# Optimization experiments

Measured on AMD Instinct MI355X. Metric: run time of the kernel, lower is better.

## Reference

```python
import jax, jax.numpy as jnp
import numpy as np

B, NPTS, DIM, BOOK, NC = 64, 1024, 256, 2048, 16
EPS = 1e-10


def setup_inputs() -> dict:
    key = jax.random.key(0)
    k1, k2, k3, k4 = jax.random.split(key, 4)
    return {
        "z": jax.random.normal(k1, (B, NPTS, DIM), dtype=jnp.float32),
        "c_probs": jax.random.uniform(k2, (B, NC), dtype=jnp.float32),
        "log_param_q": jnp.zeros((1,), dtype=jnp.float32),
        "book": jax.random.normal(k3, (BOOK, DIM), dtype=jnp.float32),
        "mu": jax.random.normal(k4, (NC, NPTS, DIM), dtype=jnp.float32),
        "temperature": 1,
        "is_train": 1,
    }


def reference(z, c_probs, log_param_q, book, mu, temperature, is_train):
    # mixture of per-cluster offsets: [b,c] x [c,n,d] -> [b,n,d]
    mu_mix = jnp.einsum('bc,cnd->bnd', c_probs, mu)
    zp = z + mu_mix
    param_q = jnp.exp(log_param_q)
    precision_q = 0.5 / jnp.clip(param_q, 1e-10)  # shape [1]
    zf = zp.reshape(-1, DIM)  # [b*npts, dim]
    # squared euclidean distance via ||z||^2 + ||e||^2 - 2 z e^T
    dist = (jnp.sum(zf * zf, axis=-1, keepdims=True)
            + jnp.sum(book * book, axis=-1)
            - 2.0 * zf @ book.T)
    logits = -dist * precision_q  # [b*npts, book_size]
    # gumbel-softmax sample (fixed key for determinism)
    U = jax.random.uniform(jax.random.key(42), logits.shape, dtype=logits.dtype)
    g = -jnp.log(-jnp.log(U + EPS) + EPS)
    encodings = jax.nn.softmax((logits + g) / temperature, axis=-1)
    zq = encodings @ book  # [b*npts, dim]
    return (zq.reshape(B, -1, DIM), precision_q, logits.reshape(B, -1, BOOK), mu_mix)
```

## Files before the change

kernel.cpp:

```cpp
#include <hip/hip_runtime.h>
#include <stdint.h>

#define BB     64
#define NPTS   1024
#define DIM    256
#define BOOKN  2048
#define NC     16
#define NROWS  (BB*NPTS)
#define HALF_N 67108864u
#define HALF_ROWS 32768

#define OFF_PQ ((size_t)NROWS*DIM)
#define OFF_LG (OFF_PQ + 1)
#define OFF_MM (OFF_LG + (size_t)NROWS*BOOKN)

#define WS_RN 2048
#define WS_PQ (2048 + NROWS)
#define WS_BF 67592
#define WS_MX (WS_BF + (BOOKN*DIM)/2)
#define WS_FUSED_BYTES ((size_t)(WS_MX + NROWS) * 4)

#if defined(__has_builtin)
# if __has_builtin(__builtin_amdgcn_logf)
#  define FAST_LOG2(x) __builtin_amdgcn_logf(x)
# endif
# if __has_builtin(__builtin_amdgcn_exp2f)
#  define FAST_EXP2(x) __builtin_amdgcn_exp2f(x)
# endif
#endif
#ifndef FAST_LOG2
# define FAST_LOG2(x) log2f(x)
#endif
#ifndef FAST_EXP2
# define FAST_EXP2(x) exp2f(x)
#endif

typedef unsigned short u16;
typedef short s8v  __attribute__((ext_vector_type(8)));
typedef float f32x4 __attribute__((ext_vector_type(4)));
typedef u16  u16x4 __attribute__((ext_vector_type(4)));
typedef u16  u16x8 __attribute__((ext_vector_type(8)));

__device__ __forceinline__ u16 f2bf(float x){
  uint32_t u = __float_as_uint(x);
  return (u16)((u + 0x7fffu + ((u >> 16) & 1u)) >> 16);
}
__device__ __forceinline__ float bf2f(u16 b){
  return __uint_as_float(((uint32_t)b) << 16);
}

__device__ __forceinline__ uint32_t mf_map(float f){
  uint32_t b = __float_as_uint(f);
  return (b & 0x80000000u) ? ~b : (b | 0x80000000u);
}
__device__ __forceinline__ float mf_unmap(uint32_t u){
  uint32_t b = (u & 0x80000000u) ? (u ^ 0x80000000u) : ~u;
  return __uint_as_float(b);
}

__device__ __forceinline__ uint32_t rotl32(uint32_t x, int r){
  return (x << r) | (x >> (32 - r));
}

__device__ __forceinline__ void threefry_0_42(uint32_t x0, uint32_t x1,
                                              uint32_t& o0, uint32_t& o1){
  const uint32_t ks0 = 0u;
  const uint32_t ks1 = 42u;
  const uint32_t ks2 = 0u ^ 42u ^ 0x1BD11BDAu;
  x0 += ks0; x1 += ks1;
#define TF_R(r) { x0 += x1; x1 = rotl32(x1, r); x1 ^= x0; }
  TF_R(13) TF_R(15) TF_R(26) TF_R(6)
  x0 += ks1; x1 += ks2 + 1u;
  TF_R(17) TF_R(29) TF_R(16) TF_R(24)
  x0 += ks2; x1 += ks0 + 2u;
  TF_R(13) TF_R(15) TF_R(26) TF_R(6)
  x0 += ks0; x1 += ks1 + 3u;
  TF_R(17) TF_R(29) TF_R(16) TF_R(24)
  x0 += ks1; x1 += ks2 + 4u;
  TF_R(13) TF_R(15) TF_R(26) TF_R(6)
  x0 += ks2; x1 += ks0 + 5u;
#undef TF_R
  o0 = x0; o1 = x1;
}

__global__ __launch_bounds__(256) void k_prep(const float* __restrict__ book,
    const float* __restrict__ lpq, float* __restrict__ bn,
    float* __restrict__ ws_pq, float* __restrict__ pq_out,
    unsigned int* __restrict__ wsMax)
{
  __shared__ float red[4];
  const int j = blockIdx.x, t = threadIdx.x;
  const int gid = j*256 + t;
  if (wsMax != nullptr && gid < NROWS) wsMax[gid] = 0u;
  float v = book[(size_t)j*DIM + t];
  float s = v*v;
  #pragma unroll
  for (int o = 32; o; o >>= 1) s += __shfl_down(s, o, 64);
  const int wv = t >> 6, ln = t & 63;
  if (ln == 0) red[wv] = s;
  __syncthreads();
  if (t == 0){
    bn[j] = red[0] + red[1] + red[2] + red[3];
    if (j == 0){
      float pq = fmaxf(expf(lpq[0]), 1e-10f);
      float prec = 0.5f / pq;
      ws_pq[0] = prec;
      pq_out[0] = prec;
    }
  }
}

__global__ __launch_bounds__(256) void k_bookf(const float* __restrict__ book,
                                               u16* __restrict__ bookF,
                                               u16* __restrict__ bookR)
{
  const int tid = blockIdx.x*256 + threadIdx.x;
  {
    const int l  = tid & 63;
    const int dt = (tid >> 6) & 15;
    const int jc = tid >> 10;
    const int d  = dt*16 + (l & 15);
    const int jb = jc*32 + (l >> 4)*8;
    u16x8 v;
    #pragma unroll
    for (int e = 0; e < 8; ++e) v[e] = f2bf(book[(size_t)(jb + e)*DIM + d]);
    *(u16x8*)&bookF[(size_t)tid*8] = v;
  }
  {
    const int rr = tid >> 5;
    const int cc = (tid & 31) * 8;
    const float4 f0 = *(const float4*)&book[(size_t)rr*DIM + cc];
    const float4 f1 = *(const float4*)&book[(size_t)rr*DIM + cc + 4];
    u16x8 wv;
    wv[0] = f2bf(f0.x); wv[1] = f2bf(f0.y); wv[2] = f2bf(f0.z); wv[3] = f2bf(f0.w);
    wv[4] = f2bf(f1.x); wv[5] = f2bf(f1.y); wv[6] = f2bf(f1.z); wv[7] = f2bf(f1.w);
    *(u16x8*)&bookR[(size_t)rr*DIM + cc] = wv;
  }
}

__global__ __launch_bounds__(256) void k_mix(const float* __restrict__ z,
    const float* __restrict__ cp, const float* __restrict__ mu,
    u16* __restrict__ zpBF, float* __restrict__ mm, float* __restrict__ rn)
{
  __shared__ float s_cp[BB*NC];
  const int n  = blockIdx.x;
  const int t  = threadIdx.x;
  const int wv = t >> 6, ln = t & 63;
  for (int e = t; e < BB*NC; e += 256) s_cp[e] = cp[e];
  const int d0 = ln*4;
  float4 muv[NC];
  #pragma unroll
  for (int c = 0; c < NC; ++c)
    muv[c] = *(const float4*)&mu[(size_t)(c*NPTS + n)*DIM + d0];
  __syncthreads();
  const int b0 = blockIdx.y*32 + wv*8;
  #pragma unroll 2
  for (int bb = 0; bb < 8; ++bb){
    const int b = b0 + bb;
    const size_t idx = ((size_t)(b*NPTS + n))*DIM + d0;
    const float4 z4 = *(const float4*)&z[idx];
    float4 m4 = {0.f, 0.f, 0.f, 0.f};
    #pragma unroll
    for (int c = 0; c < NC; ++c){
      const float wgt = s_cp[b*NC + c];
      m4.x = fmaf(wgt, muv[c].x, m4.x);
      m4.y = fmaf(wgt, muv[c].y, m4.y);
      m4.z = fmaf(wgt, muv[c].z, m4.z);
      m4.w = fmaf(wgt, muv[c].w, m4.w);
    }
    float4 zp4;
    zp4.x = z4.x + m4.x; zp4.y = z4.y + m4.y;
    zp4.z = z4.z + m4.z; zp4.w = z4.w + m4.w;
    *(float4*)&mm[idx] = m4;
    u16x4 zb;
    zb[0] = f2bf(zp4.x); zb[1] = f2bf(zp4.y);
    zb[2] = f2bf(zp4.z); zb[3] = f2bf(zp4.w);
    *(u16x4*)&zpBF[idx] = zb;
    float s = zp4.x*zp4.x + zp4.y*zp4.y + zp4.z*zp4.z + zp4.w*zp4.w;
    #pragma unroll
    for (int o = 32; o; o >>= 1) s += __shfl_down(s, o, 64);
    if (ln == 0) rn[b*NPTS + n] = s;
  }
}

__global__ __launch_bounds__(256) void k_logits(const u16* __restrict__ zpBF,
    const u16* __restrict__ bookR, const float* __restrict__ rn,
    const float* __restrict__ bn, const float* __restrict__ ws_pq,
    float* __restrict__ logits, unsigned int* __restrict__ wsMax)
{
  __shared__ u16 sA[128*72];
  __shared__ u16 sB[128*72];
  const int t  = threadIdx.x;
  const int l  = t & 63;
  const int w  = t >> 6;
  const int i0 = blockIdx.y * 128;
  const int j0 = blockIdx.x * 128;
  const int wr = (w >> 1) * 64;
  const int wc = (w & 1) * 64;
  const int ll = l & 15, lh = l >> 4;

  f32x4 acc[4][4];
  #pragma unroll
  for (int m = 0; m < 4; ++m)
    #pragma unroll
    for (int n = 0; n < 4; ++n)
      acc[m][n] = (f32x4){0.f, 0.f, 0.f, 0.f};

  for (int k0 = 0; k0 < DIM; k0 += 64){
    #pragma unroll
    for (int e = 0; e < 4; ++e){
      const int idx = e*256 + t;
      const int r   = idx >> 3;
      const int c8  = (idx & 7) * 8;
      *(u16x8*)&sA[r*72 + c8] =
          *(const u16x8*)&zpBF[(size_t)(i0 + r)*DIM + k0 + c8];
      *(u16x8*)&sB[r*72 + c8] =
          *(const u16x8*)&bookR[(size_t)(j0 + r)*DIM + k0 + c8];
    }
    __syncthreads();
    #pragma unroll
    for (int kk = 0; kk < 2; ++kk){
      s8v aF[4], bF[4];
      #pragma unroll
      for (int m = 0; m < 4; ++m)
        aF[m] = *(const s8v*)&sA[(wr + m*16 + ll)*72 + kk*32 + lh*8];
      #pragma unroll
      for (int n = 0; n < 4; ++n)
        bF[n] = *(const s8v*)&sB[(wc + n*16 + ll)*72 + kk*32 + lh*8];
      #pragma unroll
      for (int m = 0; m < 4; ++m)
        #pragma unroll
        for (int n = 0; n < 4; ++n)
          acc[m][n] = __builtin_amdgcn_mfma_f32_16x16x32_bf16(aF[m], bF[n], acc[m][n], 0, 0, 0);
    }
    __syncthreads();
  }

  const float pq = ws_pq[0];
  float bnv[4];
  #pragma unroll
  for (int n = 0; n < 4; ++n) bnv[n] = bn[j0 + wc + n*16 + ll];
  #pragma unroll
  for (int m = 0; m < 4; ++m){
    #pragma unroll
    for (int r = 0; r < 4; ++r){
      const int i = i0 + wr + m*16 + lh*4 + r;
      const float rni = rn[i];
      const size_t base = (size_t)i*BOOKN + j0 + wc + ll;
      float vmax = -3.4e38f;
      #pragma unroll
      for (int n = 0; n < 4; ++n){
        const float val = -pq * (rni + bnv[n] - 2.0f*acc[m][n][r]);
        logits[base + n*16] = val;
        vmax = fmaxf(vmax, val);
      }
      if (wsMax != nullptr){
        #pragma unroll
        for (int o = 1; o < 16; o <<= 1)
          vmax = fmaxf(vmax, __shfl_xor(vmax, o, 64));
        if (ll == 0) atomicMax(&wsMax[i], mf_map(vmax));
      }
    }
  }
}

__global__ __launch_bounds__(256) void k_zq(const float* __restrict__ logits,
    const u16* __restrict__ bookF, const int* __restrict__ temp,
    const unsigned int* __restrict__ wsMax, float* __restrict__ zq)
{
  __shared__ u16 sP[64*40];
  __shared__ float sM[64];
  __shared__ float sS[64][8];
  __shared__ float sInv[64];
  const int t  = threadIdx.x;
  const int i0 = blockIdx.x * 32;
  const float tinv = 1.0f / (float)temp[0];
  const float sc = tinv * 1.44269504f;

  if (wsMax != nullptr){
    if (t < 64){
      const int gi = (t < 32) ? (i0 + t) : (i0 + t - 32 + HALF_ROWS);
      sM[t] = mf_unmap(wsMax[gi]) + 17.0f;
    }
  } else {
    const int wv = t >> 6, ln = t & 63;
    for (int rr = 0; rr < 16; ++rr){
      const int r = wv*16 + rr;
      const int gi = (r < 32) ? (i0 + r) : (i0 + r - 32 + HALF_ROWS);
      const float* row = logits + (size_t)gi*BOOKN;
      float mx = -3.4e38f;
      #pragma unroll 4
      for (int e = 0; e < 32; ++e) mx = fmaxf(mx, row[e*64 + ln]);
      #pragma unroll
      for (int o = 32; o; o >>= 1) mx = fmaxf(mx, __shfl_down(mx, o, 64));
      if (ln == 0) sM[r] = mx + 17.0f;
    }
  }
  __syncthreads();

  const int w   = t >> 6;
  const int l   = t & 63;
  const int ll  = l & 15, lh = l >> 4;
  const int srA = t >> 3;
  const int sj0 = (t & 7) * 4;
  const int giA = i0 + srA;
  const float mA = sM[srA];
  const float mB = sM[srA + 32];
  const float* rowA = logits + (size_t)giA*BOOKN;
  const float* rowB = logits + (size_t)(giA + HALF_ROWS)*BOOKN;

  f32x4 acc[4][4];
  #pragma unroll
  for (int m = 0; m < 4; ++m)
    #pragma unroll
    for (int n = 0; n < 4; ++n)
      acc[m][n] = (f32x4){0.f, 0.f, 0.f, 0.f};
  float sumA = 0.f, sumB = 0.f;

  for (int jc = 0; jc < 64; ++jc){
    const int jbase = jc*32 + sj0;
    const float4 lA4 = *(const float4*)(rowA + jbase);
    const float4 lB4 = *(const float4*)(rowB + jbase);
    const float la[4] = {lA4.x, lA4.y, lA4.z, lA4.w};
    const float lb[4] = {lB4.x, lB4.y, lB4.z, lB4.w};
    #pragma unroll
    for (int e = 0; e < 4; ++e){
      const uint32_t p = (uint32_t)(giA*BOOKN + jbase + e);
      uint32_t o0, o1;
      threefry_0_42(p, p + HALF_N, o0, o1);
      const float uA = __uint_as_float((o0 >> 9) | 0x3f800000u) - 1.0f;
      const float uB = __uint_as_float((o1 >> 9) | 0x3f800000u) - 1.0f;
      const float wAv = fmaf(-0.69314718f, FAST_LOG2(uA + 1e-10f), 1e-10f);
      const float wBv = fmaf(-0.69314718f, FAST_LOG2(uB + 1e-10f), 1e-10f);
      const float eAv = ((la[e] - mA) - 0.69314718f*FAST_LOG2(wAv)) * sc;
      const float eBv = ((lb[e] - mB) - 0.69314718f*FAST_LOG2(wBv)) * sc;
      const u16 pa = f2bf(FAST_EXP2(eAv));
      const u16 pb = f2bf(FAST_EXP2(eBv));
      sP[srA*40 + sj0 + e]        = pa;
      sP[(srA + 32)*40 + sj0 + e] = pb;
      sumA += bf2f(pa);
      sumB += bf2f(pb);
    }
    s8v bF[4];
    #pragma unroll
    for (int n = 0; n < 4; ++n)
      bF[n] = *(const s8v*)&bookF[((size_t)(jc*16 + w*4 + n)*64 + l)*8];
    __syncthreads();
    s8v aF[4];
    #pragma unroll
    for (int m = 0; m < 4; ++m)
      aF[m] = *(const s8v*)&sP[(m*16 + ll)*40 + lh*8];
    #pragma unroll
    for (int n = 0; n < 4; ++n)
      #pragma unroll
      for (int m = 0; m < 4; ++m)
        acc[m][n] = __builtin_amdgcn_mfma_f32_16x16x32_bf16(aF[m], bF[n], acc[m][n], 0, 0, 0);
    __syncthreads();
  }

  sS[srA][t & 7]      = sumA;
  sS[srA + 32][t & 7] = sumB;
  __syncthreads();
  if (t < 64){
    float s = 0.f;
    #pragma unroll
    for (int e = 0; e < 8; ++e) s += sS[t][e];
    sInv[t] = 1.0f / s;
  }
  __syncthreads();

  #pragma unroll
  for (int m = 0; m < 4; ++m){
    #pragma unroll
    for (int r = 0; r < 4; ++r){
      const int lr = m*16 + lh*4 + r;
      const int gi = (lr < 32) ? (i0 + lr) : (i0 + lr - 32 + HALF_ROWS);
      const float inv = sInv[lr];
      #pragma unroll
      for (int n = 0; n < 4; ++n)
        zq[(size_t)gi*DIM + w*64 + n*16 + ll] = acc[m][n][r] * inv;
    }
  }
}

extern "C" void kernel_launch(void* const* d_in, const int* in_sizes, int n_in,
                              void* d_out, int out_size, void* d_ws, size_t ws_size,
                              hipStream_t stream)
{
  (void)in_sizes; (void)n_in; (void)out_size;
  const float* z    = (const float*)d_in[0];
  const float* cp   = (const float*)d_in[1];
  const float* lpq  = (const float*)d_in[2];
  const float* book = (const float*)d_in[3];
  const float* mu   = (const float*)d_in[4];
  const int*   temp = (const int*)d_in[5];

  float* out = (float*)d_out;
  float* zq  = out;
  float* pqo = out + OFF_PQ;
  float* lg  = out + OFF_LG;
  float* mm  = out + OFF_MM;

  u16* zpBF  = (u16*)zq;
  u16* bookR = (u16*)zq + (size_t)NROWS*DIM;

  float* ws    = (float*)d_ws;
  float* bn    = ws;
  float* rn    = ws + WS_RN;
  float* wpq   = ws + WS_PQ;
  u16*   bookF = (u16*)(ws + WS_BF);
  unsigned int* wsMax = (ws_size >= WS_FUSED_BYTES)
                      ? (unsigned int*)(ws + WS_MX) : nullptr;

  hipLaunchKernelGGL(k_prep,   dim3(BOOKN), dim3(256), 0, stream,
                     book, lpq, bn, wpq, pqo, wsMax);
  hipLaunchKernelGGL(k_bookf,  dim3(256), dim3(256), 0, stream,
                     book, bookF, bookR);
  hipLaunchKernelGGL(k_mix,    dim3(NPTS, 2), dim3(256), 0, stream,
                     z, cp, mu, zpBF, mm, rn);
  hipLaunchKernelGGL(k_logits, dim3(BOOKN/128, NROWS/128), dim3(256), 0, stream,
                     zpBF, bookR, rn, bn, wpq, lg, wsMax);
  hipLaunchKernelGGL(k_zq,     dim3(HALF_ROWS/32), dim3(256), 0, stream,
                     lg, bookF, temp, wsMax, zq);
}
```

Baseline: 1.223 ms.

## Fuse logits GEMM, gumbel softmax and codebook GEMM into one kernel

Adds a fused kernel in which each block owns 64 rows. It computes the distance logits with MFMA against a fragment-packed bf16 codebook and writes them out while tracking the row max. A second pass recomputes the logits in LDS, applies the Gumbel noise and exp, and accumulates encodings@book directly, so the large logits tensor never has to be read back. The cost is computing the logits GEMM twice per block, and the path only runs when the workspace is large enough for the extra packed codebook.

```diff
diff --git a/kernel.cpp b/kernel.cpp
--- a/kernel.cpp
+++ b/kernel.cpp
@@ -18,7 +18,9 @@
 #define WS_PQ (2048 + NROWS)
 #define WS_BF 67592
 #define WS_MX (WS_BF + (BOOKN*DIM)/2)
+#define WS_BQ 329736
 #define WS_FUSED_BYTES ((size_t)(WS_MX + NROWS) * 4)
+#define WS_A_BYTES ((size_t)(WS_BQ + (BOOKN*DIM)/2) * 4)
 
 #if defined(__has_builtin)
 # if __has_builtin(__builtin_amdgcn_logf)
@@ -111,8 +113,7 @@
 }
 
 __global__ __launch_bounds__(256) void k_bookf(const float* __restrict__ book,
-                                               u16* __restrict__ bookF,
-                                               u16* __restrict__ bookR)
+    u16* __restrict__ bookF, u16* __restrict__ bookR, u16* __restrict__ bookQ)
 {
   const int tid = blockIdx.x*256 + threadIdx.x;
   {
@@ -126,7 +127,7 @@
     for (int e = 0; e < 8; ++e) v[e] = f2bf(book[(size_t)(jb + e)*DIM + d]);
     *(u16x8*)&bookF[(size_t)tid*8] = v;
   }
-  {
+  if (bookR != nullptr){
     const int rr = tid >> 5;
     const int cc = (tid & 31) * 8;
     const float4 f0 = *(const float4*)&book[(size_t)rr*DIM + cc];
@@ -135,6 +136,19 @@
     wv[0] = f2bf(f0.x); wv[1] = f2bf(f0.y); wv[2] = f2bf(f0.z); wv[3] = f2bf(f0.w);
     wv[4] = f2bf(f1.x); wv[5] = f2bf(f1.y); wv[6] = f2bf(f1.z); wv[7] = f2bf(f1.w);
     *(u16x8*)&bookR[(size_t)rr*DIM + cc] = wv;
+  }
+  if (bookQ != nullptr){
+    const int l  = tid & 63;
+    const int ks = (tid >> 6) & 7;
+    const int jt = tid >> 9;
+    const int row = jt*16 + (l & 15);
+    const int d0  = ks*32 + (l >> 4)*8;
+    const float4 f0 = *(const float4*)&book[(size_t)row*DIM + d0];
+    const float4 f1 = *(const float4*)&book[(size_t)row*DIM + d0 + 4];
+    u16x8 v;
+    v[0] = f2bf(f0.x); v[1] = f2bf(f0.y); v[2] = f2bf(f0.z); v[3] = f2bf(f0.w);
+    v[4] = f2bf(f1.x); v[5] = f2bf(f1.y); v[6] = f2bf(f1.z); v[7] = f2bf(f1.w);
+    *(u16x8*)&bookQ[(size_t)tid*8] = v;
   }
 }
 
@@ -172,14 +186,208 @@
     zp4.x = z4.x + m4.x; zp4.y = z4.y + m4.y;
     zp4.z = z4.z + m4.z; zp4.w = z4.w + m4.w;
     *(float4*)&mm[idx] = m4;
-    u16x4 zb;
-    zb[0] = f2bf(zp4.x); zb[1] = f2bf(zp4.y);
-    zb[2] = f2bf(zp4.z); zb[3] = f2bf(zp4.w);
-    *(u16x4*)&zpBF[idx] = zb;
+    if (zpBF != nullptr){
+      u16x4 zb;
+      zb[0] = f2bf(zp4.x); zb[1] = f2bf(zp4.y);
+      zb[2] = f2bf(zp4.z); zb[3] = f2bf(zp4.w);
+      *(u16x4*)&zpBF[idx] = zb;
+    }
     float s = zp4.x*zp4.x + zp4.y*zp4.y + zp4.z*zp4.z + zp4.w*zp4.w;
     #pragma unroll
     for (int o = 32; o; o >>= 1) s += __shfl_down(s, o, 64);
     if (ln == 0) rn[b*NPTS + n] = s;
+  }
+}
+
+#define SLP 36
+__global__ __launch_bounds__(256) void k_fused(const float* __restrict__ z,
+    const float* __restrict__ mm, const float* __restrict__ rn,
+    const float* __restrict__ bn, const float* __restrict__ ws_pq,
+    const u16* __restrict__ bookQ, const u16* __restrict__ bookF,
+    const int* __restrict__ temp, float* __restrict__ logits,
+    float* __restrict__ zq)
+{
+  __shared__ u16 sQ[2][8192];
+  __shared__ float sL[64*SLP];
+  __shared__ u16 sP[64*40];
+  __shared__ float sM[64];
+  __shared__ float sS[64][8];
+  __shared__ float sInv[64];
+
+  const int t  = threadIdx.x;
+  const int w  = t >> 6;
+  const int l  = t & 63;
+  const int ll = l & 15, lh = l >> 4;
+  const int i0p = blockIdx.x * 32;
+  const float pq = ws_pq[0];
+  const float tinv = 1.0f / (float)temp[0];
+  const float sc = tinv * 1.44269504f;
+
+  const int sArow = w*16 + ll;
+  const int giA_r = (sArow < 32) ? (i0p + sArow) : (i0p + sArow - 32 + HALF_ROWS);
+  s8v aF[8];
+  #pragma unroll
+  for (int ks = 0; ks < 8; ++ks){
+    const size_t base = (size_t)giA_r*DIM + ks*32 + lh*8;
+    const float4 z0 = *(const float4*)&z[base];
+    const float4 z1 = *(const float4*)&z[base + 4];
+    const float4 m0 = *(const float4*)&mm[base];
+    const float4 m1 = *(const float4*)&mm[base + 4];
+    s8v v;
+    v[0] = f2bf(z0.x + m0.x); v[1] = f2bf(z0.y + m0.y);
+    v[2] = f2bf(z0.z + m0.z); v[3] = f2bf(z0.w + m0.w);
+    v[4] = f2bf(z1.x + m1.x); v[5] = f2bf(z1.y + m1.y);
+    v[6] = f2bf(z1.z + m1.z); v[7] = f2bf(z1.w + m1.w);
+    aF[ks] = v;
+  }
+  float rnv[4]; int giC[4];
+  #pragma unroll
+  for (int r = 0; r < 4; ++r){
+    const int s = w*16 + lh*4 + r;
+    giC[r] = (s < 32) ? (i0p + s) : (i0p + s - 32 + HALF_ROWS);
+    rnv[r] = rn[giC[r]];
+  }
+
+  float vmax[4] = {-3.4e38f, -3.4e38f, -3.4e38f, -3.4e38f};
+  for (int jc = 0; jc < 64; ++jc){
+    u16* q = sQ[jc & 1];
+    #pragma unroll
+    for (int e = 0; e < 4; ++e){
+      const int off = (e*256 + t)*8;
+      *(u16x8*)&q[off] = *(const u16x8*)&bookQ[(size_t)jc*8192 + off];
+    }
+    __syncthreads();
+    f32x4 accS[2];
+    accS[0] = (f32x4){0.f,0.f,0.f,0.f};
+    accS[1] = (f32x4){0.f,0.f,0.f,0.f};
+    #pragma unroll
+    for (int n = 0; n < 2; ++n)
+      #pragma unroll
+      for (int ks = 0; ks < 8; ++ks)
+        accS[n] = __builtin_amdgcn_mfma_f32_16x16x32_bf16(
+            aF[ks], *(const s8v*)&q[((n*8 + ks)*64 + l)*8], accS[n], 0, 0, 0);
+    const float bnv[2] = { bn[jc*32 + ll], bn[jc*32 + 16 + ll] };
+    #pragma unroll
+    for (int n = 0; n < 2; ++n)
+      #pragma unroll
+      for (int r = 0; r < 4; ++r){
+        const float val = -pq * (rnv[r] + bnv[n] - 2.0f*accS[n][r]);
+        logits[(size_t)giC[r]*BOOKN + jc*32 + n*16 + ll] = val;
+        vmax[r] = fmaxf(vmax[r], val);
+      }
+  }
+  #pragma unroll
+  for (int r = 0; r < 4; ++r){
+    float m = vmax[r];
+    #pragma unroll
+    for (int o = 1; o < 16; o <<= 1) m = fmaxf(m, __shfl_xor(m, o, 64));
+    if (ll == 0) sM[w*16 + lh*4 + r] = m + 17.0f;
+  }
+  __syncthreads();
+
+  const int srA = t >> 3;
+  const int sj0 = (t & 7) * 4;
+  const int giA = i0p + srA;
+  const float mA = sM[srA];
+  const float mB = sM[srA + 32];
+
+  f32x4 acc[4][4];
+  #pragma unroll
+  for (int m = 0; m < 4; ++m)
+    #pragma unroll
+    for (int n = 0; n < 4; ++n)
+      acc[m][n] = (f32x4){0.f, 0.f, 0.f, 0.f};
+  float sumA = 0.f, sumB = 0.f;
+
+  for (int jc = 0; jc < 64; ++jc){
+    u16* q = sQ[jc & 1];
+    #pragma unroll
+    for (int e = 0; e < 4; ++e){
+      const int off = (e*256 + t)*8;
+      *(u16x8*)&q[off] = *(const u16x8*)&bookQ[(size_t)jc*8192 + off];
+    }
+    __syncthreads();
+    f32x4 accS[2];
+    accS[0] = (f32x4){0.f,0.f,0.f,0.f};
+    accS[1] = (f32x4){0.f,0.f,0.f,0.f};
+    #pragma unroll
+    for (int n = 0; n < 2; ++n)
+      #pragma unroll
+      for (int ks = 0; ks < 8; ++ks)
+        accS[n] = __builtin_amdgcn_mfma_f32_16x16x32_bf16(
+            aF[ks], *(const s8v*)&q[((n*8 + ks)*64 + l)*8], accS[n], 0, 0, 0);
+    const float bnv[2] = { bn[jc*32 + ll], bn[jc*32 + 16 + ll] };
+    #pragma unroll
+    for (int n = 0; n < 2; ++n)
+      #pragma unroll
+      for (int r = 0; r < 4; ++r)
+        sL[(w*16 + lh*4 + r)*SLP + n*16 + ll] =
+            -pq * (rnv[r] + bnv[n] - 2.0f*accS[n][r]);
+    __syncthreads();
+
+    {
+      const float4 lA4 = *(const float4*)&sL[srA*SLP + sj0];
+      const float4 lB4 = *(const float4*)&sL[(srA + 32)*SLP + sj0];
+      const float la[4] = {lA4.x, lA4.y, lA4.z, lA4.w};
+      const float lb[4] = {lB4.x, lB4.y, lB4.z, lB4.w};
+      const int jbase = jc*32 + sj0;
+      #pragma unroll
+      for (int e = 0; e < 4; ++e){
+        const uint32_t p = (uint32_t)(giA*BOOKN + jbase + e);
+        uint32_t o0, o1;
+        threefry_0_42(p, p + HALF_N, o0, o1);
+        const float uA = __uint_as_float((o0 >> 9) | 0x3f800000u) - 1.0f;
+        const float uB = __uint_as_float((o1 >> 9) | 0x3f800000u) - 1.0f;
+        const float wAv = fmaf(-0.69314718f, FAST_LOG2(uA + 1e-10f), 1e-10f);
+        const float wBv = fmaf(-0.69314718f, FAST_LOG2(uB + 1e-10f), 1e-10f);
+        const float eAv = ((la[e] - mA) - 0.69314718f*FAST_LOG2(wAv)) * sc;
+        const float eBv = ((lb[e] - mB) - 0.69314718f*FAST_LOG2(wBv)) * sc;
+        const u16 pa = f2bf(FAST_EXP2(eAv));
+        const u16 pb = f2bf(FAST_EXP2(eBv));
+        sP[srA*40 + sj0 + e]        = pa;
+        sP[(srA + 32)*40 + sj0 + e] = pb;
+        sumA += bf2f(pa);
+        sumB += bf2f(pb);
+      }
+    }
+    s8v bF[4];
+    #pragma unroll
+    for (int n = 0; n < 4; ++n)
+      bF[n] = *(const s8v*)&bookF[((size_t)(jc*16 + w*4 + n)*64 + l)*8];
+    __syncthreads();
+    s8v aP[4];
+    #pragma unroll
+    for (int m = 0; m < 4; ++m)
+      aP[m] = *(const s8v*)&sP[(m*16 + ll)*40 + lh*8];
+    #pragma unroll
+    for (int n = 0; n < 4; ++n)
+      #pragma unroll
+      for (int m = 0; m < 4; ++m)
+        acc[m][n] = __builtin_amdgcn_mfma_f32_16x16x32_bf16(aP[m], bF[n], acc[m][n], 0, 0, 0);
+  }
+
+  sS[srA][t & 7]      = sumA;
+  sS[srA + 32][t & 7] = sumB;
+  __syncthreads();
+  if (t < 64){
+    float s = 0.f;
+    #pragma unroll
+    for (int e = 0; e < 8; ++e) s += sS[t][e];
+    sInv[t] = 1.0f / s;
+  }
+  __syncthreads();
+
+  #pragma unroll
+  for (int m = 0; m < 4; ++m){
+    #pragma unroll
+    for (int r = 0; r < 4; ++r){
+      const int lr = m*16 + lh*4 + r;
+      const int gi = (lr < 32) ? (i0p + lr) : (i0p + lr - 32 + HALF_ROWS);
+      const float inv = sInv[lr];
+      #pragma unroll
+      for (int n = 0; n < 4; ++n)
+        zq[(size_t)gi*DIM + w*64 + n*16 + ll] = acc[m][n][r] * inv;
+    }
   }
 }
 
@@ -212,10 +420,8 @@
       const int idx = e*256 + t;
       const int r   = idx >> 3;
       const int c8  = (idx & 7) * 8;
-      *(u16x8*)&sA[r*72 + c8] =
-          *(const u16x8*)&zpBF[(size_t)(i0 + r)*DIM + k0 + c8];
-      *(u16x8*)&sB[r*72 + c8] =
-          *(const u16x8*)&bookR[(size_t)(j0 + r)*DIM + k0 + c8];
+      *(u16x8*)&sA[r*72 + c8] = *(const u16x8*)&zpBF[(size_t)(i0 + r)*DIM + k0 + c8];
+      *(u16x8*)&sB[r*72 + c8] = *(const u16x8*)&bookR[(size_t)(j0 + r)*DIM + k0 + c8];
     }
     __syncthreads();
     #pragma unroll
@@ -401,25 +607,36 @@
   float* lg  = out + OFF_LG;
   float* mm  = out + OFF_MM;
 
-  u16* zpBF  = (u16*)zq;
-  u16* bookR = (u16*)zq + (size_t)NROWS*DIM;
-
   float* ws    = (float*)d_ws;
   float* bn    = ws;
   float* rn    = ws + WS_RN;
   float* wpq   = ws + WS_PQ;
   u16*   bookF = (u16*)(ws + WS_BF);
-  unsigned int* wsMax = (ws_size >= WS_FUSED_BYTES)
-                      ? (unsigned int*)(ws + WS_MX) : nullptr;
-
-  hipLaunchKernelGGL(k_prep,   dim3(BOOKN), dim3(256), 0, stream,
-                     book, lpq, bn, wpq, pqo, wsMax);
-  hipLaunchKernelGGL(k_bookf,  dim3(256), dim3(256), 0, stream,
-                     book, bookF, bookR);
-  hipLaunchKernelGGL(k_mix,    dim3(NPTS, 2), dim3(256), 0, stream,
-                     z, cp, mu, zpBF, mm, rn);
-  hipLaunchKernelGGL(k_logits, dim3(BOOKN/128, NROWS/128), dim3(256), 0, stream,
-                     zpBF, bookR, rn, bn, wpq, lg, wsMax);
-  hipLaunchKernelGGL(k_zq,     dim3(HALF_ROWS/32), dim3(256), 0, stream,
-                     lg, bookF, temp, wsMax, zq);
-}
+
+  if (ws_size >= WS_A_BYTES){
+    u16* bookQ = (u16*)(ws + WS_BQ);
+    hipLaunchKernelGGL(k_prep,  dim3(BOOKN), dim3(256), 0, stream,
+                       book, lpq, bn, wpq, pqo, (unsigned int*)nullptr);
+    hipLaunchKernelGGL(k_bookf, dim3(256), dim3(256), 0, stream,
+                       book, bookF, (u16*)nullptr, bookQ);
+    hipLaunchKernelGGL(k_mix,   dim3(NPTS, 2), dim3(256), 0, stream,
+                       z, cp, mu, (u16*)nullptr, mm, rn);
+    hipLaunchKernelGGL(k_fused, dim3(HALF_ROWS/32), dim3(256), 0, stream,
+                       z, mm, rn, bn, wpq, bookQ, bookF, temp, lg, zq);
+  } else {
+    u16* zpBF  = (u16*)zq;
+    u16* bookR = (u16*)zq + (size_t)NROWS*DIM;
+    unsigned int* wsMax = (ws_size >= WS_FUSED_BYTES)
+                        ? (unsigned int*)(ws + WS_MX) : nullptr;
+    hipLaunchKernelGGL(k_prep,   dim3(BOOKN), dim3(256), 0, stream,
+                       book, lpq, bn, wpq, pqo, wsMax);
+    hipLaunchKernelGGL(k_bookf,  dim3(256), dim3(256), 0, stream,
+                       book, bookF, bookR, (u16*)nullptr);
+    hipLaunchKernelGGL(k_mix,    dim3(NPTS, 2), dim3(256), 0, stream,
+                       z, cp, mu, zpBF, mm, rn);
+    hipLaunchKernelGGL(k_logits, dim3(BOOKN/128, NROWS/128), dim3(256), 0, stream,
+                       zpBF, bookR, rn, bn, wpq, lg, wsMax);
+    hipLaunchKernelGGL(k_zq,     dim3(HALF_ROWS/32), dim3(256), 0, stream,
+                       lg, bookF, temp, wsMax, zq);
+  }
+}
```

Result: slower. 1.304 ms (+6.7%).
